# Performance work log

Measured on AMD Instinct MI355X. Metric: run time of the kernel, lower is better.

Reference implementation:

```python
import jax, jax.numpy as jnp
import numpy as np

EMBED_DIM = 1024
HEAD_DIM = 64


def setup_inputs() -> dict:
    key = jax.random.key(0)
    ks = jax.random.split(key, 7)
    B, S = 4, 2048
    s = 1.0 / np.sqrt(EMBED_DIM)
    h = jax.random.normal(ks[0], (B, S, EMBED_DIM), dtype=jnp.float32)
    Wq = jax.random.normal(ks[1], (EMBED_DIM, HEAD_DIM), dtype=jnp.float32) * s
    bq = jax.random.normal(ks[2], (HEAD_DIM,), dtype=jnp.float32) * 0.01
    Wk = jax.random.normal(ks[3], (EMBED_DIM, HEAD_DIM), dtype=jnp.float32) * s
    bk = jax.random.normal(ks[4], (HEAD_DIM,), dtype=jnp.float32) * 0.01
    Wv = jax.random.normal(ks[5], (EMBED_DIM, HEAD_DIM), dtype=jnp.float32) * s
    bv = jax.random.normal(ks[6], (HEAD_DIM,), dtype=jnp.float32) * 0.01
    return {"h": h, "Wq": Wq, "bq": bq, "Wk": Wk, "bk": bk, "Wv": Wv, "bv": bv}


def reference(h, Wq, bq, Wk, bk, Wv, bv):
    # Linear projections: h [B,S,E] -> q,k [B,S,D]
    q = jnp.einsum("bse,ed->bsd", h, Wq) + bq
    k = jnp.einsum("bse,ed->bsd", h, Wk) + bk
    v = jnp.einsum("bse,ed->bsd", h, Wv) + bv  # computed but UNUSED (faithful to source)
    del v
    scale = 1.0 / jnp.sqrt(jnp.asarray(HEAD_DIM, dtype=q.dtype))
    # scores [B, Sq, Sk]
    scores = jnp.einsum("bqd,bkd->bqk", q, k) * scale
    # NOTE: source uses softmax over dim=1 (query axis), not the key axis
    weights = jax.nn.softmax(scores, axis=1)
    # NOTE: source passes h (not v) as the value tensor
    out = jnp.einsum("bqk,bke->bqe", weights, h)  # [B, Sq, E]
    return out
```

## Files before the change

### kernel.cpp

```cpp
#include <hip/hip_runtime.h>
#include <hip/hip_bf16.h>
#include <math.h>

#define EMBED 1024
#define HDIM  64
#define BATCH 4
#define SEQ   2048

typedef __attribute__((ext_vector_type(8))) short short8;
typedef __attribute__((ext_vector_type(4))) float f32x4;
typedef unsigned int u32;
typedef unsigned short u16;

static __device__ __forceinline__ u16 f2bf(float f) {
    union { float f; u32 u; } v; v.f = f;
    u32 r = v.u + 0x7fffu + ((v.u >> 16) & 1u);
    return (u16)(r >> 16);
}

static __device__ __forceinline__ void gload_lds16(const u16* g, u16* l) {
    __builtin_amdgcn_global_load_lds(
        (const __attribute__((address_space(1))) u32*)g,
        (__attribute__((address_space(3))) u32*)l, 16, 0, 0);
}

__global__ __launch_bounds__(256) void wt_kernel(
    const float* __restrict__ Wq, const float* __restrict__ Wk,
    u16* __restrict__ WqT, u16* __restrict__ WkT)
{
    __shared__ float tile[64][65];
    const float* W = blockIdx.y ? Wk : Wq;
    u16* WT = blockIdx.y ? WkT : WqT;
    int e0 = blockIdx.x * 64;
    int t = threadIdx.x, c = t & 63, r4 = t >> 6;
    for (int r = r4; r < 64; r += 4)
        tile[r][c] = W[(size_t)(e0 + r) * HDIM + c];
    __syncthreads();
    for (int d = r4; d < 64; d += 4)
        WT[(size_t)d * EMBED + e0 + c] = f2bf(tile[c][d]);
}

__global__ __launch_bounds__(256) void proj_kernel(
    const float* __restrict__ h, const u16* __restrict__ WqT, const u16* __restrict__ WkT,
    const float* __restrict__ bq, const float* __restrict__ bk,
    u16* __restrict__ Qbf, u16* __restrict__ Kbf)
{
    __shared__ u16 hs[2][16][136];
    int b = blockIdx.x >> 7, s0 = (blockIdx.x & 127) * 16;
    int t = threadIdx.x, lane = t & 63, w = t >> 6;
    int l15 = lane & 15, quad = lane >> 4;
    int pj = w >> 1, nh = (w & 1) * 32;
    const float* hb = h + ((size_t)b * SEQ + s0) * EMBED;
    const u16* Wp = pj ? WkT : WqT;
    int r = t >> 4, c4 = (t & 15) * 4;

    f32x4 pre0 = *(const f32x4*)(hb + (size_t)r * EMBED + c4);
    f32x4 pre1 = *(const f32x4*)(hb + (size_t)r * EMBED + 64 + c4);
    f32x4 accA[2], accB[2];
    accA[0] = accA[1] = accB[0] = accB[1] = (f32x4){0.f, 0.f, 0.f, 0.f};

    const u16* Wrow0 = Wp + (size_t)(nh + l15) * EMBED;
    const u16* Wrow1 = Wp + (size_t)(nh + 16 + l15) * EMBED;

    short8 cw[8];
#pragma unroll
    for (int i = 0; i < 4; i++) {
        cw[i]     = *(const short8*)(Wrow0 + i * 32 + quad * 8);
        cw[4 + i] = *(const short8*)(Wrow1 + i * 32 + quad * 8);
    }

    for (int it = 0; it < 8; ++it) {
        int ec = it * 128, buf = it & 1;
        uint2 pk;
        pk.x = (u32)f2bf(pre0[0]) | ((u32)f2bf(pre0[1]) << 16);
        pk.y = (u32)f2bf(pre0[2]) | ((u32)f2bf(pre0[3]) << 16);
        *(uint2*)&hs[buf][r][c4] = pk;
        pk.x = (u32)f2bf(pre1[0]) | ((u32)f2bf(pre1[1]) << 16);
        pk.y = (u32)f2bf(pre1[2]) | ((u32)f2bf(pre1[3]) << 16);
        *(uint2*)&hs[buf][r][64 + c4] = pk;
        __syncthreads();

        if (it + 1 < 8) {
            pre0 = *(const f32x4*)(hb + (size_t)r * EMBED + ec + 128 + c4);
            pre1 = *(const f32x4*)(hb + (size_t)r * EMBED + ec + 192 + c4);
        }
        short8 nw[8];
#pragma unroll
        for (int i = 0; i < 8; i++) nw[i] = cw[i];
        if (it + 1 < 8) {
#pragma unroll
            for (int i = 0; i < 4; i++) {
                nw[i]     = *(const short8*)(Wrow0 + ec + 128 + i * 32 + quad * 8);
                nw[4 + i] = *(const short8*)(Wrow1 + ec + 128 + i * 32 + quad * 8);
            }
        }

        short8 a0 = *(const short8*)&hs[buf][l15][quad * 8];
        short8 a1 = *(const short8*)&hs[buf][l15][32 + quad * 8];
        short8 a2 = *(const short8*)&hs[buf][l15][64 + quad * 8];
        short8 a3 = *(const short8*)&hs[buf][l15][96 + quad * 8];
        accA[0] = __builtin_amdgcn_mfma_f32_16x16x32_bf16(a0, cw[0], accA[0], 0, 0, 0);
        accA[1] = __builtin_amdgcn_mfma_f32_16x16x32_bf16(a0, cw[4], accA[1], 0, 0, 0);
        accB[0] = __builtin_amdgcn_mfma_f32_16x16x32_bf16(a1, cw[1], accB[0], 0, 0, 0);
        accB[1] = __builtin_amdgcn_mfma_f32_16x16x32_bf16(a1, cw[5], accB[1], 0, 0, 0);
        accA[0] = __builtin_amdgcn_mfma_f32_16x16x32_bf16(a2, cw[2], accA[0], 0, 0, 0);
        accA[1] = __builtin_amdgcn_mfma_f32_16x16x32_bf16(a2, cw[6], accA[1], 0, 0, 0);
        accB[0] = __builtin_amdgcn_mfma_f32_16x16x32_bf16(a3, cw[3], accB[0], 0, 0, 0);
        accB[1] = __builtin_amdgcn_mfma_f32_16x16x32_bf16(a3, cw[7], accB[1], 0, 0, 0);
#pragma unroll
        for (int i = 0; i < 8; i++) cw[i] = nw[i];
    }

    const float* bias = pj ? bk : bq;
    float scale = pj ? 1.0f : 0.125f;
    u16* outp = pj ? Kbf : Qbf;
    float bv0 = bias[nh + l15], bv1 = bias[nh + 16 + l15];
#pragma unroll
    for (int rr = 0; rr < 4; rr++) {
        size_t row = (size_t)b * SEQ + s0 + quad * 4 + rr;
        outp[row * HDIM + nh + l15]      = f2bf((accA[0][rr] + accB[0][rr] + bv0) * scale);
        outp[row * HDIM + nh + 16 + l15] = f2bf((accA[1][rr] + accB[1][rr] + bv1) * scale);
    }
}

__global__ __launch_bounds__(256) void sw_kernel(
    const u16* __restrict__ Qbf, const u16* __restrict__ Kbf,
    u16* __restrict__ Wmat, float* __restrict__ invl)
{
    __shared__ float sl[4][16];
    int b = blockIdx.y;
    int k0 = blockIdx.x * 16;
    int t = threadIdx.x, lane = t & 63, w = t >> 6;
    int l15 = lane & 15, quad = lane >> 4;
    const u16* Qb = Qbf + (size_t)b * SEQ * HDIM;
    const u16* Kb = Kbf + (size_t)b * SEQ * HDIM;
    u16* Wb = Wmat + (size_t)b * SEQ * SEQ;
    short8 kf0 = *(const short8*)(Kb + (size_t)(k0 + l15) * HDIM + quad * 8);
    short8 kf1 = *(const short8*)(Kb + (size_t)(k0 + l15) * HDIM + 32 + quad * 8);
    f32x4 lacc = {0.f, 0.f, 0.f, 0.f};
    int qs = w * 512;
    const u16* qpa = Qb + (size_t)(qs + l15) * HDIM;
    const u16* qpb = Qb + (size_t)(qs + 16 + l15) * HDIM;
    short8 cf0a = *(const short8*)(qpa + quad * 8);
    short8 cf1a = *(const short8*)(qpa + 32 + quad * 8);
    short8 cf0b = *(const short8*)(qpb + quad * 8);
    short8 cf1b = *(const short8*)(qpb + 32 + quad * 8);

    for (int q0 = qs; q0 < qs + 512; q0 += 32) {
        short8 nf0a = cf0a, nf1a = cf1a, nf0b = cf0b, nf1b = cf1b;
        if (q0 + 32 < qs + 512) {
            const u16* na = Qb + (size_t)(q0 + 32 + l15) * HDIM;
            const u16* nb = Qb + (size_t)(q0 + 48 + l15) * HDIM;
            nf0a = *(const short8*)(na + quad * 8);
            nf1a = *(const short8*)(na + 32 + quad * 8);
            nf0b = *(const short8*)(nb + quad * 8);
            nf1b = *(const short8*)(nb + 32 + quad * 8);
        }
        f32x4 aa = {0.f, 0.f, 0.f, 0.f}, ab = {0.f, 0.f, 0.f, 0.f};
        aa = __builtin_amdgcn_mfma_f32_16x16x32_bf16(kf0, cf0a, aa, 0, 0, 0);
        ab = __builtin_amdgcn_mfma_f32_16x16x32_bf16(kf0, cf0b, ab, 0, 0, 0);
        aa = __builtin_amdgcn_mfma_f32_16x16x32_bf16(kf1, cf1a, aa, 0, 0, 0);
        ab = __builtin_amdgcn_mfma_f32_16x16x32_bf16(kf1, cf1b, ab, 0, 0, 0);
        float e0 = __expf(aa[0]), e1 = __expf(aa[1]);
        float e2 = __expf(aa[2]), e3 = __expf(aa[3]);
        float g0 = __expf(ab[0]), g1 = __expf(ab[1]);
        float g2 = __expf(ab[2]), g3 = __expf(ab[3]);
        lacc[0] += e0 + g0; lacc[1] += e1 + g1;
        lacc[2] += e2 + g2; lacc[3] += e3 + g3;
        uint2 pa, pb;
        pa.x = (u32)f2bf(e0) | ((u32)f2bf(e1) << 16);
        pa.y = (u32)f2bf(e2) | ((u32)f2bf(e3) << 16);
        pb.x = (u32)f2bf(g0) | ((u32)f2bf(g1) << 16);
        pb.y = (u32)f2bf(g2) | ((u32)f2bf(g3) << 16);
        *(uint2*)(Wb + (size_t)(q0 + l15) * SEQ + k0 + quad * 4) = pa;
        *(uint2*)(Wb + (size_t)(q0 + 16 + l15) * SEQ + k0 + quad * 4) = pb;
        cf0a = nf0a; cf1a = nf1a; cf0b = nf0b; cf1b = nf1b;
    }
#pragma unroll
    for (int m = 1; m <= 8; m <<= 1) {
        lacc[0] += __shfl_xor(lacc[0], m, 64);
        lacc[1] += __shfl_xor(lacc[1], m, 64);
        lacc[2] += __shfl_xor(lacc[2], m, 64);
        lacc[3] += __shfl_xor(lacc[3], m, 64);
    }
    if (l15 == 0) {
        sl[w][quad * 4 + 0] = lacc[0];
        sl[w][quad * 4 + 1] = lacc[1];
        sl[w][quad * 4 + 2] = lacc[2];
        sl[w][quad * 4 + 3] = lacc[3];
    }
    __syncthreads();
    if (t < 16)
        invl[b * SEQ + k0 + t] =
            1.0f / ((sl[0][t] + sl[1][t]) + (sl[2][t] + sl[3][t]));
}

__global__ __launch_bounds__(256) void tscale_kernel(
    const float* __restrict__ h, const float* __restrict__ invl,
    u16* __restrict__ hT)
{
    __shared__ float tile[64][65];
    int b  = blockIdx.z;
    int s0 = blockIdx.x * 64, e0 = blockIdx.y * 64;
    int t = threadIdx.x, c = t & 63, r4 = t >> 6;
    const float* hb = h + (size_t)b * SEQ * EMBED;
    for (int r = r4; r < 64; r += 4)
        tile[r][c] = hb[(size_t)(s0 + r) * EMBED + e0 + c];
    __syncthreads();
    float il = invl[b * SEQ + s0 + c];
    u16* hTb = hT + (size_t)b * EMBED * SEQ;
    for (int er = r4; er < 64; er += 4)
        hTb[(size_t)(e0 + er) * SEQ + s0 + c] = f2bf(tile[c][er] * il);
}

__global__ __launch_bounds__(512, 2) void out_gemm_kernel(
    const u16* __restrict__ Wmat, const u16* __restrict__ hT, float* __restrict__ out)
{
    __shared__ u16 As[3][256 * 64];
    __shared__ u16 Bs[3][128 * 64];
    int b = blockIdx.z;
    int q0 = blockIdx.x * 256, e0 = blockIdx.y * 128;
    int t = threadIdx.x, lane = t & 63, w = t >> 6;
    int l15 = lane & 15, quad = lane >> 4;
    const u16* Wb  = Wmat + (size_t)b * SEQ * SEQ;
    const u16* hTb = hT + (size_t)b * EMBED * SEQ;
    int wm = w >> 1, wn = w & 1;
    int wq = wm * 64, we = wn * 64;

    f32x4 acc[4][4];
#pragma unroll
    for (int qi = 0; qi < 4; qi++)
#pragma unroll
        for (int ej = 0; ej < 4; ej++) acc[qi][ej] = (f32x4){0.f, 0.f, 0.f, 0.f};

    int st_rl = lane >> 3;
    int st_pc = lane & 7;

#define STAGE(si, k0)                                                          \
    {                                                                          \
        _Pragma("unroll")                                                      \
        for (int ld = 0; ld < 4; ld++) {                                       \
            int rowb = w * 32 + ld * 8;                                        \
            int row  = rowb + st_rl;                                           \
            int cg   = st_pc ^ (row & 7);            \
            gload_lds16(Wb + (size_t)(q0 + row) * SEQ + (k0) + cg * 8,         \
                        &As[si][rowb * 64] + lane * 8);                        \
        }                                                                      \
        _Pragma("unroll")                                                      \
        for (int ld = 0; ld < 2; ld++) {                                       \
            int rowb = w * 16 + ld * 8;                                        \
            int row  = rowb + st_rl;                                           \
            int cg   = st_pc ^ (row & 7);                                      \
            gload_lds16(hTb + (size_t)(e0 + row) * SEQ + (k0) + cg * 8,        \
                        &Bs[si][rowb * 64] + lane * 8);                        \
        }                                                                      \
    }

    STAGE(0, 0)
    STAGE(1, 64)

    for (int kt = 0; kt < 32; ++kt) {
        int s = kt % 3;
        if (kt == 31) { asm volatile("s_waitcnt vmcnt(0)" ::: "memory"); }
        else          { asm volatile("s_waitcnt vmcnt(6)" ::: "memory"); }
        __builtin_amdgcn_s_barrier();
        asm volatile("" ::: "memory");
        if (kt + 2 < 32) {
            int s2 = (kt + 2) % 3;
            STAGE(s2, (kt + 2) * 64)
        }
        asm volatile("" ::: "memory");

        const u16* Ab = &As[s][0];
        const u16* Bb = &Bs[s][0];
        short8 bfr[2][4], af[2][4];
#pragma unroll
        for (int kf = 0; kf < 2; kf++)
#pragma unroll
            for (int j = 0; j < 4; j++) {
                int rb  = we + j * 16 + l15;
                int pcb = (kf * 4 + quad) ^ (rb & 7);
                bfr[kf][j] = *(const short8*)(Bb + rb * 64 + pcb * 8);
            }
#pragma unroll
        for (int kf = 0; kf < 2; kf++)
#pragma unroll
            for (int i = 0; i < 4; i++) {
                int ra  = wq + i * 16 + l15;
                int pca = (kf * 4 + quad) ^ (ra & 7);
                af[kf][i] = *(const short8*)(Ab + ra * 64 + pca * 8);
            }
        __builtin_amdgcn_s_setprio(1);
#pragma unroll
        for (int kf = 0; kf < 2; kf++)
#pragma unroll
            for (int qi = 0; qi < 4; qi++)
#pragma unroll
                for (int ej = 0; ej < 4; ej++)
                    acc[qi][ej] = __builtin_amdgcn_mfma_f32_16x16x32_bf16(
                        af[kf][qi], bfr[kf][ej], acc[qi][ej], 0, 0, 0);
        __builtin_amdgcn_s_setprio(0);
    }
#undef STAGE

    float* outb = out + (size_t)b * SEQ * EMBED;
#pragma unroll
    for (int qi = 0; qi < 4; qi++)
#pragma unroll
        for (int ej = 0; ej < 4; ej++)
#pragma unroll
            for (int r = 0; r < 4; r++)
                outb[(size_t)(q0 + wq + qi * 16 + quad * 4 + r) * EMBED
                     + e0 + we + ej * 16 + l15] = acc[qi][ej][r];
}

extern "C" void kernel_launch(void* const* d_in, const int* in_sizes, int n_in,
                              void* d_out, int out_size, void* d_ws, size_t ws_size,
                              hipStream_t stream) {
    (void)in_sizes; (void)n_in; (void)out_size; (void)ws_size;
    const float* h  = (const float*)d_in[0];
    const float* Wq = (const float*)d_in[1];
    const float* bq = (const float*)d_in[2];
    const float* Wk = (const float*)d_in[3];
    const float* bk = (const float*)d_in[4];
    float* out = (float*)d_out;

    char* ws = (char*)d_ws;
    u16*   Qbf  = (u16*)(ws);
    u16*   Kbf  = (u16*)(ws + (1ull << 20));
    u16*   hT   = (u16*)(ws + (2ull << 20));
    float* invl = (float*)(ws + (18ull << 20));
    u16*   WqT  = (u16*)(ws + (18ull << 20) + (128ull << 10));
    u16*   WkT  = (u16*)(ws + (18ull << 20) + (256ull << 10));
    u16*   Wmat = (u16*)(ws + (19ull << 20));

    hipLaunchKernelGGL(wt_kernel, dim3(16, 2), dim3(256), 0, stream, Wq, Wk, WqT, WkT);
    hipLaunchKernelGGL(proj_kernel, dim3(512), dim3(256), 0, stream,
                       h, WqT, WkT, bq, bk, Qbf, Kbf);
    hipLaunchKernelGGL(sw_kernel, dim3(128, 4), dim3(256), 0, stream,
                       Qbf, Kbf, Wmat, invl);
    hipLaunchKernelGGL(tscale_kernel, dim3(32, 16, 4), dim3(256), 0, stream,
                       h, invl, hT);
    hipLaunchKernelGGL(out_gemm_kernel, dim3(8, 8, 4), dim3(512), 0, stream,
                       Wmat, hT, out);
}
```

Before: 183.8 us.

## Split GEMM k-tile into two half-phases interleaving global loads with MFMA

Restructures the main loop of the weights×h GEMM so each 64-wide k-tile is processed in two halves. Each half loads its LDS fragments, issues half of the next-next stage's global-to-LDS loads, then runs 16 MFMAs behind a sched_barrier. The vmcnt wait moves to the end of the iteration. The aim is to spread memory issue across the compute phases and shrink register use for fragments, at the cost of extra s_barriers per iteration.

Result: faster. 178.2 us (-3.1%).

```diff
diff --git a/kernel.cpp b/kernel.cpp
--- a/kernel.cpp
+++ b/kernel.cpp
@@ -236,72 +236,91 @@
     int st_rl = lane >> 3;
     int st_pc = lane & 7;
 
-#define STAGE(si, k0)                                                          \
+#define STAGE_A(si, k0, ld)                                                    \
+    {                                                                          \
+        int rowb = w * 32 + (ld) * 8;                                          \
+        int row  = rowb + st_rl;                                               \
+        int cg   = st_pc ^ (row & 7);                \
+        gload_lds16(Wb + (size_t)(q0 + row) * SEQ + (k0) + cg * 8,             \
+                    &As[si][rowb * 64] + lane * 8);                            \
+    }
+#define STAGE_B(si, k0, ld)                                                    \
+    {                                                                          \
+        int rowb = w * 16 + (ld) * 8;                                          \
+        int row  = rowb + st_rl;                                               \
+        int cg   = st_pc ^ (row & 7);                                          \
+        gload_lds16(hTb + (size_t)(e0 + row) * SEQ + (k0) + cg * 8,            \
+                    &Bs[si][rowb * 64] + lane * 8);                            \
+    }
+
+#define LDFRAGS(kf)                                                            \
     {                                                                          \
         _Pragma("unroll")                                                      \
-        for (int ld = 0; ld < 4; ld++) {                                       \
-            int rowb = w * 32 + ld * 8;                                        \
-            int row  = rowb + st_rl;                                           \
-            int cg   = st_pc ^ (row & 7);            \
-            gload_lds16(Wb + (size_t)(q0 + row) * SEQ + (k0) + cg * 8,         \
-                        &As[si][rowb * 64] + lane * 8);                        \
+        for (int i = 0; i < 4; i++) {                                          \
+            int ra  = wq + i * 16 + l15;                                       \
+            int pca = ((kf) * 4 + quad) ^ (ra & 7);                            \
+            af[i] = *(const short8*)(Ab + ra * 64 + pca * 8);                  \
         }                                                                      \
         _Pragma("unroll")                                                      \
-        for (int ld = 0; ld < 2; ld++) {                                       \
-            int rowb = w * 16 + ld * 8;                                        \
-            int row  = rowb + st_rl;                                           \
-            int cg   = st_pc ^ (row & 7);                                      \
-            gload_lds16(hTb + (size_t)(e0 + row) * SEQ + (k0) + cg * 8,        \
-                        &Bs[si][rowb * 64] + lane * 8);                        \
+        for (int j = 0; j < 4; j++) {                                          \
+            int rb  = we + j * 16 + l15;                                       \
+            int pcb = ((kf) * 4 + quad) ^ (rb & 7);                            \
+            bfr[j] = *(const short8*)(Bb + rb * 64 + pcb * 8);                 \
         }                                                                      \
     }
 
-    STAGE(0, 0)
-    STAGE(1, 64)
+#define MFMA16                                                                 \
+    {                                                                          \
+        _Pragma("unroll")                                                      \
+        for (int qi = 0; qi < 4; qi++)                                         \
+            _Pragma("unroll")                                                  \
+            for (int ej = 0; ej < 4; ej++)                                     \
+                acc[qi][ej] = __builtin_amdgcn_mfma_f32_16x16x32_bf16(         \
+                    af[qi], bfr[ej], acc[qi][ej], 0, 0, 0);                    \
+    }
+
+    STAGE_A(0, 0, 0) STAGE_A(0, 0, 1) STAGE_A(0, 0, 2) STAGE_A(0, 0, 3)
+    STAGE_B(0, 0, 0) STAGE_B(0, 0, 1)
+    STAGE_A(1, 64, 0) STAGE_A(1, 64, 1) STAGE_A(1, 64, 2) STAGE_A(1, 64, 3)
+    STAGE_B(1, 64, 0) STAGE_B(1, 64, 1)
+    asm volatile("s_waitcnt vmcnt(6)" ::: "memory");
+    __builtin_amdgcn_s_barrier();
 
     for (int kt = 0; kt < 32; ++kt) {
         int s = kt % 3;
-        if (kt == 31) { asm volatile("s_waitcnt vmcnt(0)" ::: "memory"); }
-        else          { asm volatile("s_waitcnt vmcnt(6)" ::: "memory"); }
-        __builtin_amdgcn_s_barrier();
-        asm volatile("" ::: "memory");
-        if (kt + 2 < 32) {
-            int s2 = (kt + 2) % 3;
-            STAGE(s2, (kt + 2) * 64)
-        }
-        asm volatile("" ::: "memory");
-
         const u16* Ab = &As[s][0];
         const u16* Bb = &Bs[s][0];
-        short8 bfr[2][4], af[2][4];
-#pragma unroll
-        for (int kf = 0; kf < 2; kf++)
-#pragma unroll
-            for (int j = 0; j < 4; j++) {
-                int rb  = we + j * 16 + l15;
-                int pcb = (kf * 4 + quad) ^ (rb & 7);
-                bfr[kf][j] = *(const short8*)(Bb + rb * 64 + pcb * 8);
-            }
-#pragma unroll
-        for (int kf = 0; kf < 2; kf++)
-#pragma unroll
-            for (int i = 0; i < 4; i++) {
-                int ra  = wq + i * 16 + l15;
-                int pca = (kf * 4 + quad) ^ (ra & 7);
-                af[kf][i] = *(const short8*)(Ab + ra * 64 + pca * 8);
-            }
+        int s2 = (kt + 2) % 3;
+        int k2 = (kt + 2) * 64;
+        bool st = (kt + 2) < 32;
+        short8 af[4], bfr[4];
+
+        LDFRAGS(0)
+        if (st) { STAGE_A(s2, k2, 0) STAGE_A(s2, k2, 1) STAGE_B(s2, k2, 0) }
+        __builtin_amdgcn_s_barrier();
+        asm volatile("s_waitcnt lgkmcnt(0)" ::: "memory");
+        __builtin_amdgcn_sched_barrier(0);
         __builtin_amdgcn_s_setprio(1);
-#pragma unroll
-        for (int kf = 0; kf < 2; kf++)
-#pragma unroll
-            for (int qi = 0; qi < 4; qi++)
-#pragma unroll
-                for (int ej = 0; ej < 4; ej++)
-                    acc[qi][ej] = __builtin_amdgcn_mfma_f32_16x16x32_bf16(
-                        af[kf][qi], bfr[kf][ej], acc[qi][ej], 0, 0, 0);
+        MFMA16
         __builtin_amdgcn_s_setprio(0);
-    }
-#undef STAGE
+        __builtin_amdgcn_s_barrier();
+
+        LDFRAGS(1)
+        if (st) { STAGE_A(s2, k2, 2) STAGE_A(s2, k2, 3) STAGE_B(s2, k2, 1) }
+        __builtin_amdgcn_s_barrier();
+        asm volatile("s_waitcnt lgkmcnt(0)" ::: "memory");
+        __builtin_amdgcn_sched_barrier(0);
+        __builtin_amdgcn_s_setprio(1);
+        MFMA16
+        __builtin_amdgcn_s_setprio(0);
+        if (kt < 30)       { asm volatile("s_waitcnt vmcnt(6)" ::: "memory"); }
+        else if (kt == 30) { asm volatile("s_waitcnt vmcnt(0)" ::: "memory"); }
+        __builtin_amdgcn_s_barrier();
+    }
+#undef STAGE_A
+#undef STAGE_B
+#undef LDFRAGS
+#undef MFMA16
 
     float* outb = out + (size_t)b * SEQ * EMBED;
 #pragma unroll
```
